# Performance work log

Measured on AMD Instinct MI355X. Metric: run time of the kernel, lower is better.

Reference implementation:

```python
import jax, jax.numpy as jnp
from jax import lax
import numpy as np

D = 512          # dim_embedding
VW = 50000       # word vocab
VC = 256         # char vocab
N = 4096         # number of words
L = 32           # chars per word


def setup_inputs() -> dict:
    key = jax.random.key(0)
    ks = jax.random.split(key, 12)
    inp = {
        "words": jax.random.randint(ks[0], (N,), 0, VW),
        "words_in_char": jax.random.randint(ks[1], (N, L), 0, VC),
        "word_emb": jax.random.normal(ks[2], (VW, D), jnp.float32) * 0.05,
        "chr_emb": jax.random.normal(ks[3], (VC, D), jnp.float32) * 0.05,
        "conv_chr_w": jax.random.normal(ks[4], (D, D, 3), jnp.float32) * 0.02,
        "conv_chr_b": jax.random.normal(ks[5], (D,), jnp.float32) * 0.02,
        "conv_sent_w": jax.random.normal(ks[6], (2 * D, 2 * D, 3), jnp.float32) * 0.02,
        "conv_sent_b": jax.random.normal(ks[7], (2 * D,), jnp.float32) * 0.02,
        "lin1_w": jax.random.normal(ks[8], (4 * D, 2 * D), jnp.float32) * 0.02,
        "lin1_b": jax.random.normal(ks[9], (4 * D,), jnp.float32) * 0.02,
        "lin2_w": jax.random.normal(ks[10], (2, 4 * D), jnp.float32) * 0.02,
        "lin2_b": jax.random.normal(ks[11], (2,), jnp.float32) * 0.02,
    }
    return inp


def reference(words, words_in_char, word_emb, chr_emb, conv_chr_w, conv_chr_b,
              conv_sent_w, conv_sent_b, lin1_w, lin1_b, lin2_w, lin2_b):
    # padding_idx=0 -> row 0 of embeddings is zero
    we = word_emb.at[0].set(0.0)
    ce = chr_emb.at[0].set(0.0)

    n, l = words_in_char.shape
    d = we.shape[1]

    v_word = we[words]                      # [N, D]

    emb_c = ce[words_in_char]               # [N, L, D]
    # FAITHFUL to original: reshape (not transpose) of [L, D] into [D, L]
    x = emb_c.reshape(n, d, l)              # [N, D, L]
    y = lax.conv_general_dilated(
        x, conv_chr_w, window_strides=(1,), padding=[(1, 1)],
        dimension_numbers=("NCH", "OIH", "NCH"))
    y = y + conv_chr_b[None, :, None]       # [N, D, L]
    v_wch = jnp.max(y, axis=2)              # [N, D]  (max-pool over char positions)

    u = jnp.concatenate([v_word, v_wch], axis=1)   # [N, 2D]
    # conv_sentence acts on length-1 sequences with pad=1: only the center
    # kernel tap touches real data -> equivalent to a matmul with w[:, :, 1]
    r = u @ conv_sent_w[:, :, 1].T + conv_sent_b   # [N, 2D]
    r = jnp.max(r, axis=0)                          # [2D] max over words

    h = jnp.tanh(r @ lin1_w.T + lin1_b)             # [4D]
    return h @ lin2_w.T + lin2_b                    # [2]
```

## Files before the change

kernel.cpp:

```cpp
#include <hip/hip_runtime.h>
#include <hip/hip_fp16.h>

typedef _Float16 f16;
typedef __attribute__((ext_vector_type(8))) _Float16 f16x8;
typedef __attribute__((ext_vector_type(4))) float f32x4;

#define WS_CET   0u
#define WS_WC    262144u
#define WS_W1    1835008u
#define WS_U     3932160u
#define WS_PART  12320768u
#define WS_RMAX  12451840u
#define WS_H     12455936u

__global__ __launch_bounds__(512) void k0_ceT(const float* __restrict__ ce,
                                              f16* __restrict__ ceT) {
  int c = blockIdx.x;
  int t = threadIdx.x;
  int m = t >> 5, l = t & 31;
  float v = (c == 0) ? 0.f : ce[c * 512 + m * 32 + l];
  ceT[c * 512 + l * 16 + m] = (f16)v;
}

__global__ __launch_bounds__(256) void k0_wc(const float* __restrict__ w,
                                             f16* __restrict__ Wc) {
  int e = blockIdx.x * 256 + threadIdx.x;
  int k = e >> 18, rem = e & 262143;
  int o = rem >> 9, i = rem & 511;
  Wc[e] = (f16)w[(o * 512 + i) * 3 + k];
}

__global__ __launch_bounds__(256) void k0_w1(const float* __restrict__ w,
                                             f16* __restrict__ W1) {
  int e = blockIdx.x * 256 + threadIdx.x;
  int o = e >> 10, i = e & 1023;
  W1[e] = (f16)w[(o * 1024 + i) * 3 + 1];
}

__global__ __launch_bounds__(256) void k0_u(const int* __restrict__ words,
                                            const float* __restrict__ wemb,
                                            f16* __restrict__ U) {
  int n = blockIdx.x;
  int wd = words[n];
  const float* src = wemb + (size_t)wd * 512;
  for (int i = threadIdx.x; i < 512; i += 256) {
    float v = (wd == 0) ? 0.f : src[i];
    U[n * 1024 + i] = (f16)v;
  }
}

__global__ __launch_bounds__(256) void k1_conv(
    const int* __restrict__ wic, const f16* __restrict__ Wc,
    const f16* __restrict__ ceT, const float* __restrict__ bias,
    f16* __restrict__ U)
{
  __shared__ __align__(16) f16 sA[3 * 128 * 32];
  __shared__ __align__(16) f16 sB[8 * 34 * 32];
  __shared__ int   sChar[256];
  __shared__ float sBias[128];

  const int tid = threadIdx.x;
  const int w0 = blockIdx.x * 8;
  const int o0 = blockIdx.y * 128;
  const int wid = tid >> 6, lane = tid & 63;
  const int wm = wid >> 1, wn = wid & 1;
  const int l15 = lane & 15, g4 = lane >> 4;

  sChar[tid] = wic[w0 * 32 + tid];
  if (tid < 128) sBias[tid] = bias[o0 + tid];

  f32x4 acc[4][8];
#pragma unroll
  for (int m = 0; m < 4; ++m)
#pragma unroll
    for (int n = 0; n < 8; ++n) acc[m][n] = (f32x4){0.f, 0.f, 0.f, 0.f};

  __syncthreads();

  for (int step = 0; step < 16; ++step) {
    const int i0 = step * 32, gb = step * 2;
#pragma unroll
    for (int c = tid; c < 1536; c += 256) {
      int k = c >> 9, rem = c & 511, o = rem >> 2, ch = rem & 3;
      uint4 v = *(const uint4*)(Wc + ((k * 512 + o0 + o) * 512 + i0 + ch * 8));
      *(uint4*)((char*)sA + (((k * 128 + o) * 4 + (ch ^ (o & 3))) << 4)) = v;
    }
    for (int c = tid; c < 1088; c += 256) {
      int w = c / 136, rem = c - w * 136, lp = rem >> 2, ch = rem & 3;
      uint4 v = make_uint4(0u, 0u, 0u, 0u);
      if (lp > 0 && lp < 33) {
        int cc = sChar[(w << 5) + gb + (ch >> 1)];
        v = *(const uint4*)(ceT + (cc * 512 + (lp - 1) * 16 + (ch & 1) * 8));
      }
      *(uint4*)((char*)sB + (((w * 34 + lp) * 4 + (ch ^ (lp & 3))) << 4)) = v;
    }
    __syncthreads();

#pragma unroll
    for (int k = 0; k < 3; ++k) {
      f16x8 a[4];
#pragma unroll
      for (int m = 0; m < 4; ++m) {
        int ol = wm * 64 + m * 16 + l15;
        a[m] = *(const f16x8*)((const char*)sA +
                 (((k * 128 + ol) * 4 + (g4 ^ (ol & 3))) << 4));
      }
#pragma unroll
      for (int n = 0; n < 8; ++n) {
        int w = wn * 4 + (n >> 1);
        int lp = (n & 1) * 16 + l15 + k;
        f16x8 b = *(const f16x8*)((const char*)sB +
                   (((w * 34 + lp) * 4 + (g4 ^ (lp & 3))) << 4));
#pragma unroll
        for (int m = 0; m < 4; ++m)
          acc[m][n] = __builtin_amdgcn_mfma_f32_16x16x32_f16(a[m], b, acc[m][n], 0, 0, 0);
      }
    }
    __syncthreads();
  }

#pragma unroll
  for (int m = 0; m < 4; ++m) {
    float vm[16];
#pragma unroll
    for (int wp = 0; wp < 4; ++wp)
#pragma unroll
      for (int j = 0; j < 4; ++j)
        vm[wp * 4 + j] = fmaxf(acc[m][2 * wp][j], acc[m][2 * wp + 1][j]);
#pragma unroll
    for (int off = 1; off <= 8; off <<= 1)
#pragma unroll
      for (int t = 0; t < 16; ++t)
        vm[t] = fmaxf(vm[t], __shfl_xor(vm[t], off));
    float v = vm[0];
#pragma unroll
    for (int t = 1; t < 16; ++t) v = (l15 == t) ? vm[t] : v;
    int ol = wm * 64 + m * 16 + g4 * 4 + (l15 & 3);
    int word = w0 + wn * 4 + (l15 >> 2);
    U[word * 1024 + 512 + o0 + ol] = (f16)(v + sBias[ol]);
  }
}

__global__ __launch_bounds__(256) void k2_sent(
    const f16* __restrict__ U, const f16* __restrict__ W1,
    float* __restrict__ part)
{
  __shared__ __align__(16) f16 sA[128 * 32];
  __shared__ __align__(16) f16 sB[128 * 32];
  __shared__ float sRed[2][128];

  const int tid = threadIdx.x;
  const int w0 = blockIdx.x * 128;
  const int o0 = blockIdx.y * 128;
  const int wid = tid >> 6, lane = tid & 63;
  const int wm = wid >> 1, wn = wid & 1;
  const int l15 = lane & 15, g4 = lane >> 4;

  f32x4 acc[4][4];
#pragma unroll
  for (int m = 0; m < 4; ++m)
#pragma unroll
    for (int n = 0; n < 4; ++n) acc[m][n] = (f32x4){0.f, 0.f, 0.f, 0.f};

  for (int step = 0; step < 32; ++step) {
    const int i0 = step * 32;
#pragma unroll
    for (int c = tid; c < 512; c += 256) {
      int r = c >> 2, ch = c & 3;
      uint4 va = *(const uint4*)(U + (w0 + r) * 1024 + i0 + ch * 8);
      *(uint4*)((char*)sA + ((r * 4 + (ch ^ (r & 3))) << 4)) = va;
      uint4 vb = *(const uint4*)(W1 + (o0 + r) * 1024 + i0 + ch * 8);
      *(uint4*)((char*)sB + ((r * 4 + (ch ^ (r & 3))) << 4)) = vb;
    }
    __syncthreads();
    f16x8 a[4];
#pragma unroll
    for (int m = 0; m < 4; ++m) {
      int r = wm * 64 + m * 16 + l15;
      a[m] = *(const f16x8*)((const char*)sA + ((r * 4 + (g4 ^ (r & 3))) << 4));
    }
#pragma unroll
    for (int n = 0; n < 4; ++n) {
      int r = wn * 64 + n * 16 + l15;
      f16x8 b = *(const f16x8*)((const char*)sB + ((r * 4 + (g4 ^ (r & 3))) << 4));
#pragma unroll
      for (int m = 0; m < 4; ++m)
        acc[m][n] = __builtin_amdgcn_mfma_f32_16x16x32_f16(a[m], b, acc[m][n], 0, 0, 0);
    }
    __syncthreads();
  }
#pragma unroll
  for (int n = 0; n < 4; ++n) {
    float v = -3.4e38f;
#pragma unroll
    for (int m = 0; m < 4; ++m)
#pragma unroll
      for (int j = 0; j < 4; ++j) v = fmaxf(v, acc[m][n][j]);
    v = fmaxf(v, __shfl_xor(v, 16));
    v = fmaxf(v, __shfl_xor(v, 32));
    if (lane < 16) sRed[wm][wn * 64 + n * 16 + l15] = v;
  }
  __syncthreads();
  if (tid < 128)
    part[blockIdx.x * 1024 + o0 + tid] = fmaxf(sRed[0][tid], sRed[1][tid]);
}

__global__ __launch_bounds__(256) void k3_rmax(const float* __restrict__ part,
                                               const float* __restrict__ sb,
                                               float* __restrict__ rmax) {
  int o = blockIdx.x * 256 + threadIdx.x;
  float v = -3.4e38f;
  for (int r = 0; r < 32; ++r) v = fmaxf(v, part[r * 1024 + o]);
  rmax[o] = v + sb[o];
}

__global__ __launch_bounds__(256) void k3_lin1(const float* __restrict__ w,
                                               const float* __restrict__ b,
                                               const float* __restrict__ rmax,
                                               float* __restrict__ h) {
  __shared__ float sR[1024];
  int tid = threadIdx.x;
  for (int i = tid; i < 1024; i += 256) sR[i] = rmax[i];
  __syncthreads();
  int wid = tid >> 6, lane = tid & 63;
  for (int p = 0; p < 8; ++p) {
    int j = blockIdx.x * 32 + p * 4 + wid;
    float a = 0.f;
    for (int i = lane; i < 1024; i += 64) a += w[j * 1024 + i] * sR[i];
#pragma unroll
    for (int off = 32; off >= 1; off >>= 1) a += __shfl_xor(a, off);
    if (lane == 0) h[j] = tanhf(a + b[j]);
  }
}

__global__ __launch_bounds__(256) void k3_out(const float* __restrict__ h,
                                              const float* __restrict__ w,
                                              const float* __restrict__ b,
                                              float* __restrict__ out) {
  __shared__ float red0[4], red1[4];
  int tid = threadIdx.x, wid = tid >> 6, lane = tid & 63;
  float a0 = 0.f, a1 = 0.f;
  for (int i = tid; i < 2048; i += 256) {
    float hv = h[i];
    a0 += hv * w[i];
    a1 += hv * w[2048 + i];
  }
#pragma unroll
  for (int off = 32; off >= 1; off >>= 1) {
    a0 += __shfl_xor(a0, off);
    a1 += __shfl_xor(a1, off);
  }
  if (lane == 0) { red0[wid] = a0; red1[wid] = a1; }
  __syncthreads();
  if (tid == 0) {
    out[0] = red0[0] + red0[1] + red0[2] + red0[3] + b[0];
    out[1] = red1[0] + red1[1] + red1[2] + red1[3] + b[1];
  }
}

extern "C" void kernel_launch(void* const* d_in, const int* in_sizes, int n_in,
                              void* d_out, int out_size, void* d_ws, size_t ws_size,
                              hipStream_t stream) {
  (void)in_sizes; (void)n_in; (void)out_size; (void)ws_size;
  const int*   words = (const int*)d_in[0];
  const int*   wic   = (const int*)d_in[1];
  const float* wemb  = (const float*)d_in[2];
  const float* cemb  = (const float*)d_in[3];
  const float* ccw   = (const float*)d_in[4];
  const float* ccb   = (const float*)d_in[5];
  const float* csw   = (const float*)d_in[6];
  const float* csb   = (const float*)d_in[7];
  const float* l1w   = (const float*)d_in[8];
  const float* l1b   = (const float*)d_in[9];
  const float* l2w   = (const float*)d_in[10];
  const float* l2b   = (const float*)d_in[11];
  float* out = (float*)d_out;
  char* ws = (char*)d_ws;
  f16* ceT = (f16*)(ws + WS_CET);
  f16* Wc  = (f16*)(ws + WS_WC);
  f16* W1  = (f16*)(ws + WS_W1);
  f16* U   = (f16*)(ws + WS_U);
  float* part = (float*)(ws + WS_PART);
  float* rmax = (float*)(ws + WS_RMAX);
  float* h    = (float*)(ws + WS_H);

  k0_ceT <<<dim3(256),    dim3(512), 0, stream>>>(cemb, ceT);
  k0_wc  <<<dim3(3072),   dim3(256), 0, stream>>>(ccw, Wc);
  k0_w1  <<<dim3(4096),   dim3(256), 0, stream>>>(csw, W1);
  k0_u   <<<dim3(4096),   dim3(256), 0, stream>>>(words, wemb, U);
  k1_conv<<<dim3(512, 4), dim3(256), 0, stream>>>(wic, Wc, ceT, ccb, U);
  k2_sent<<<dim3(32, 8),  dim3(256), 0, stream>>>(U, W1, part);
  k3_rmax<<<dim3(4),      dim3(256), 0, stream>>>(part, csb, rmax);
  k3_lin1<<<dim3(64),     dim3(256), 0, stream>>>(l1w, l1b, rmax, h);
  k3_out <<<dim3(1),      dim3(256), 0, stream>>>(h, l2w, l2b, out);
}
```

Baseline: 709.8 us.

## Fuse prep kernels, double-buffer conv and sentence GEMMs with direct global-to-LDS loads

Merges the four preprocessing kernels into one launch and pre-swizzles the conv weights into a tile-ordered layout. The char-conv kernel now covers 16 words per block with 8x8 MFMA tiles per wave, and the sentence GEMM uses 64-wide K steps. Both GEMMs double-buffer LDS and fill it with global_load_lds, so the next tile's loads overlap the current tile's MFMAs. The cost is more LDS and registers per block (launch bounds now allow one block per SIMD group), which lowers occupancy.

```diff
diff --git a/kernel.cpp b/kernel.cpp
--- a/kernel.cpp
+++ b/kernel.cpp
@@ -13,179 +13,211 @@
 #define WS_RMAX  12451840u
 #define WS_H     12455936u
 
-__global__ __launch_bounds__(512) void k0_ceT(const float* __restrict__ ce,
-                                              f16* __restrict__ ceT) {
-  int c = blockIdx.x;
-  int t = threadIdx.x;
-  int m = t >> 5, l = t & 31;
-  float v = (c == 0) ? 0.f : ce[c * 512 + m * 32 + l];
-  ceT[c * 512 + l * 16 + m] = (f16)v;
-}
-
-__global__ __launch_bounds__(256) void k0_wc(const float* __restrict__ w,
-                                             f16* __restrict__ Wc) {
-  int e = blockIdx.x * 256 + threadIdx.x;
-  int k = e >> 18, rem = e & 262143;
-  int o = rem >> 9, i = rem & 511;
-  Wc[e] = (f16)w[(o * 512 + i) * 3 + k];
-}
-
-__global__ __launch_bounds__(256) void k0_w1(const float* __restrict__ w,
-                                             f16* __restrict__ W1) {
-  int e = blockIdx.x * 256 + threadIdx.x;
-  int o = e >> 10, i = e & 1023;
-  W1[e] = (f16)w[(o * 1024 + i) * 3 + 1];
-}
-
-__global__ __launch_bounds__(256) void k0_u(const int* __restrict__ words,
-                                            const float* __restrict__ wemb,
-                                            f16* __restrict__ U) {
-  int n = blockIdx.x;
-  int wd = words[n];
-  const float* src = wemb + (size_t)wd * 512;
-  for (int i = threadIdx.x; i < 512; i += 256) {
-    float v = (wd == 0) ? 0.f : src[i];
-    U[n * 1024 + i] = (f16)v;
-  }
-}
-
-__global__ __launch_bounds__(256) void k1_conv(
+__device__ __forceinline__ void gload16(const void* g, void* l) {
+  __builtin_amdgcn_global_load_lds(
+      (const __attribute__((address_space(1))) unsigned int*)g,
+      (__attribute__((address_space(3))) unsigned int*)l, 16, 0, 0);
+}
+
+__global__ __launch_bounds__(256) void k0_prep(
+    const int* __restrict__ words, const float* __restrict__ wemb,
+    const float* __restrict__ cemb, const float* __restrict__ ccw,
+    const float* __restrict__ csw,
+    f16* __restrict__ ceT, f16* __restrict__ Wc, f16* __restrict__ W1,
+    f16* __restrict__ U)
+{
+  int b = blockIdx.x, tid = threadIdx.x;
+  if (b < 384) {
+    int q = b * 256 + tid;
+    int oblk = q / 24576;
+    int r = q - oblk * 24576;
+    int step = r / 1536, p = r - step * 1536;
+    int k = p >> 9, ol = (p >> 2) & 127, chp = p & 3;
+    int ch = chp ^ ((ol >> 1) & 3);
+    int o = oblk * 128 + ol, i0 = step * 32 + ch * 8;
+    f16x8 v;
+#pragma unroll
+    for (int j = 0; j < 8; ++j) v[j] = (f16)ccw[(o * 512 + i0 + j) * 3 + k];
+    *(f16x8*)(Wc + (size_t)q * 8) = v;
+  } else if (b < 4480) {
+    int e = (b - 384) * 256 + tid;
+    int o = e >> 10, i = e & 1023;
+    W1[e] = (f16)csw[(o * 1024 + i) * 3 + 1];
+  } else if (b < 4992) {
+    int e = (b - 4480) * 256 + tid;
+    int c = e >> 9, t = e & 511;
+    int m = t >> 5, l = t & 31;
+    float v = (c == 0) ? 0.f : cemb[c * 512 + m * 32 + l];
+    ceT[c * 512 + l * 16 + m] = (f16)v;
+  } else {
+    int n = b - 4992;
+    int wd = words[n];
+    const float* src = wemb + (size_t)wd * 512;
+    for (int i = tid; i < 512; i += 256)
+      U[n * 1024 + i] = (f16)((wd == 0) ? 0.f : src[i]);
+  }
+}
+
+__global__ __launch_bounds__(256, 1) void k1_conv(
     const int* __restrict__ wic, const f16* __restrict__ Wc,
     const f16* __restrict__ ceT, const float* __restrict__ bias,
     f16* __restrict__ U)
 {
-  __shared__ __align__(16) f16 sA[3 * 128 * 32];
-  __shared__ __align__(16) f16 sB[8 * 34 * 32];
-  __shared__ int   sChar[256];
+  __shared__ __align__(16) f16 sA[2][12288];
+  __shared__ __align__(16) f16 sB[2][17408];
+  __shared__ int sChar[512];
   __shared__ float sBias[128];
 
   const int tid = threadIdx.x;
-  const int w0 = blockIdx.x * 8;
-  const int o0 = blockIdx.y * 128;
+  const int w0 = blockIdx.x * 16;
+  const int oblk = blockIdx.y;
+  const int o0 = oblk * 128;
+  const int wid = tid >> 6, lane = tid & 63;
+  const int l15 = lane & 15, g4 = lane >> 4;
+
+  sChar[tid] = wic[w0 * 32 + tid];
+  sChar[tid + 256] = wic[w0 * 32 + 256 + tid];
+  if (tid < 128) sBias[tid] = bias[o0 + tid];
+  {
+    int buf = tid >> 7, rem = tid & 127, w = rem >> 3, q = rem & 7;
+    int chk = w * 136 + (q < 4 ? q : 128 + q);
+    *(uint4*)((char*)sB[buf] + (chk << 4)) = make_uint4(0, 0, 0, 0);
+  }
+  __syncthreads();
+
+  auto stgA = [&](int buf, int step) {
+    const f16* src = Wc + ((size_t)(oblk * 16 + step) * 1536 + wid * 384 + lane) * 8;
+    f16* dst = sA[buf] + wid * 3072;
+#pragma unroll
+    for (int c = 0; c < 6; ++c)
+      gload16(src + c * 512, dst + c * 512);
+  };
+  auto stgB = [&](int buf, int step) {
+#pragma unroll
+    for (int c = 0; c < 8; ++c) {
+      int wl = wid * 4 + (c >> 1), h = c & 1;
+      int lp = 1 + h * 16 + (lane >> 2);
+      int ch = (lane & 3) ^ ((lp >> 1) & 3);
+      int cc = sChar[wl * 32 + step * 2 + (ch >> 1)];
+      gload16(ceT + cc * 512 + (lp - 1) * 16 + (ch & 1) * 8,
+              sB[buf] + (wl * 136 + 4 + h * 64) * 8);
+    }
+  };
+
+  stgA(0, 0); stgB(0, 0);
+
+  f32x4 acc[8][8];
+#pragma unroll
+  for (int m = 0; m < 8; ++m)
+#pragma unroll
+    for (int n = 0; n < 8; ++n) acc[m][n] = (f32x4){0.f, 0.f, 0.f, 0.f};
+
+  __syncthreads();
+
+  for (int t = 0; t < 16; ++t) {
+    const int cur = t & 1;
+    if (t < 15) { stgA(cur ^ 1, t + 1); stgB(cur ^ 1, t + 1); }
+    const f16* A = sA[cur];
+    const f16* B = sB[cur];
+#pragma unroll
+    for (int k = 0; k < 3; ++k) {
+      f16x8 a[8];
+#pragma unroll
+      for (int m = 0; m < 8; ++m) {
+        int row = m * 16 + l15;
+        int pc = g4 ^ ((row >> 1) & 3);
+        a[m] = *(const f16x8*)(A + ((k * 128 + row) * 4 + pc) * 8);
+      }
+#pragma unroll
+      for (int n = 0; n < 8; ++n) {
+        int wl = wid * 4 + (n >> 1);
+        int lp = (n & 1) * 16 + l15 + k;
+        int pc = g4 ^ ((lp >> 1) & 3);
+        f16x8 bfr = *(const f16x8*)(B + (wl * 136 + lp * 4 + pc) * 8);
+#pragma unroll
+        for (int m = 0; m < 8; ++m)
+          acc[m][n] = __builtin_amdgcn_mfma_f32_16x16x32_f16(a[m], bfr, acc[m][n], 0, 0, 0);
+      }
+    }
+    __syncthreads();
+  }
+
+#pragma unroll
+  for (int m = 0; m < 8; ++m) {
+    float vm[16];
+#pragma unroll
+    for (int wp = 0; wp < 4; ++wp)
+#pragma unroll
+      for (int j = 0; j < 4; ++j)
+        vm[wp * 4 + j] = fmaxf(acc[m][2 * wp][j], acc[m][2 * wp + 1][j]);
+#pragma unroll
+    for (int off = 1; off <= 8; off <<= 1)
+#pragma unroll
+      for (int q = 0; q < 16; ++q)
+        vm[q] = fmaxf(vm[q], __shfl_xor(vm[q], off));
+    float v = vm[0];
+#pragma unroll
+    for (int q = 1; q < 16; ++q) v = (l15 == q) ? vm[q] : v;
+    int ol = m * 16 + g4 * 4 + (l15 & 3);
+    int word = w0 + wid * 4 + (l15 >> 2);
+    U[word * 1024 + 512 + o0 + ol] = (f16)(v + sBias[ol]);
+  }
+}
+
+__global__ __launch_bounds__(256, 1) void k2_sent(
+    const f16* __restrict__ U, const f16* __restrict__ W1,
+    float* __restrict__ part)
+{
+  __shared__ __align__(16) f16 sA[2][8192];
+  __shared__ __align__(16) f16 sB[2][8192];
+  __shared__ float sRed[2][128];
+
+  const int tid = threadIdx.x;
+  const int w0 = blockIdx.x * 128, o0 = blockIdx.y * 128;
   const int wid = tid >> 6, lane = tid & 63;
   const int wm = wid >> 1, wn = wid & 1;
   const int l15 = lane & 15, g4 = lane >> 4;
 
-  sChar[tid] = wic[w0 * 32 + tid];
-  if (tid < 128) sBias[tid] = bias[o0 + tid];
-
-  f32x4 acc[4][8];
+  auto stg = [&](int buf, int step) {
+    int i0 = step * 64;
+#pragma unroll
+    for (int c = 0; c < 4; ++c) {
+      int row = wid * 32 + c * 8 + (lane >> 3);
+      int ch = (lane & 7) ^ (row & 7);
+      gload16(U  + (size_t)(w0 + row) * 1024 + i0 + ch * 8, sA[buf] + (wid * 32 + c * 8) * 64);
+      gload16(W1 + (size_t)(o0 + row) * 1024 + i0 + ch * 8, sB[buf] + (wid * 32 + c * 8) * 64);
+    }
+  };
+
+  stg(0, 0);
+  f32x4 acc[4][4];
 #pragma unroll
   for (int m = 0; m < 4; ++m)
 #pragma unroll
-    for (int n = 0; n < 8; ++n) acc[m][n] = (f32x4){0.f, 0.f, 0.f, 0.f};
-
-  __syncthreads();
-
-  for (int step = 0; step < 16; ++step) {
-    const int i0 = step * 32, gb = step * 2;
-#pragma unroll
-    for (int c = tid; c < 1536; c += 256) {
-      int k = c >> 9, rem = c & 511, o = rem >> 2, ch = rem & 3;
-      uint4 v = *(const uint4*)(Wc + ((k * 512 + o0 + o) * 512 + i0 + ch * 8));
-      *(uint4*)((char*)sA + (((k * 128 + o) * 4 + (ch ^ (o & 3))) << 4)) = v;
-    }
-    for (int c = tid; c < 1088; c += 256) {
-      int w = c / 136, rem = c - w * 136, lp = rem >> 2, ch = rem & 3;
-      uint4 v = make_uint4(0u, 0u, 0u, 0u);
-      if (lp > 0 && lp < 33) {
-        int cc = sChar[(w << 5) + gb + (ch >> 1)];
-        v = *(const uint4*)(ceT + (cc * 512 + (lp - 1) * 16 + (ch & 1) * 8));
+    for (int n = 0; n < 4; ++n) acc[m][n] = (f32x4){0.f, 0.f, 0.f, 0.f};
+  __syncthreads();
+
+  for (int t = 0; t < 16; ++t) {
+    const int cur = t & 1;
+    if (t < 15) stg(cur ^ 1, t + 1);
+#pragma unroll
+    for (int s = 0; s < 2; ++s) {
+      f16x8 a[4];
+#pragma unroll
+      for (int m = 0; m < 4; ++m) {
+        int row = wm * 64 + m * 16 + l15;
+        int pc = (s * 4 + g4) ^ (row & 7);
+        a[m] = *(const f16x8*)(sA[cur] + row * 64 + pc * 8);
       }
-      *(uint4*)((char*)sB + (((w * 34 + lp) * 4 + (ch ^ (lp & 3))) << 4)) = v;
-    }
-    __syncthreads();
-
-#pragma unroll
-    for (int k = 0; k < 3; ++k) {
-      f16x8 a[4];
-#pragma unroll
-      for (int m = 0; m < 4; ++m) {
-        int ol = wm * 64 + m * 16 + l15;
-        a[m] = *(const f16x8*)((const char*)sA +
-                 (((k * 128 + ol) * 4 + (g4 ^ (ol & 3))) << 4));
+#pragma unroll
+      for (int n = 0; n < 4; ++n) {
+        int row = wn * 64 + n * 16 + l15;
+        int pc = (s * 4 + g4) ^ (row & 7);
+        f16x8 bfr = *(const f16x8*)(sB[cur] + row * 64 + pc * 8);
+#pragma unroll
+        for (int m = 0; m < 4; ++m)
+          acc[m][n] = __builtin_amdgcn_mfma_f32_16x16x32_f16(a[m], bfr, acc[m][n], 0, 0, 0);
       }
-#pragma unroll
-      for (int n = 0; n < 8; ++n) {
-        int w = wn * 4 + (n >> 1);
-        int lp = (n & 1) * 16 + l15 + k;
-        f16x8 b = *(const f16x8*)((const char*)sB +
-                   (((w * 34 + lp) * 4 + (g4 ^ (lp & 3))) << 4));
-#pragma unroll
-        for (int m = 0; m < 4; ++m)
-          acc[m][n] = __builtin_amdgcn_mfma_f32_16x16x32_f16(a[m], b, acc[m][n], 0, 0, 0);
-      }
-    }
-    __syncthreads();
-  }
-
-#pragma unroll
-  for (int m = 0; m < 4; ++m) {
-    float vm[16];
-#pragma unroll
-    for (int wp = 0; wp < 4; ++wp)
-#pragma unroll
-      for (int j = 0; j < 4; ++j)
-        vm[wp * 4 + j] = fmaxf(acc[m][2 * wp][j], acc[m][2 * wp + 1][j]);
-#pragma unroll
-    for (int off = 1; off <= 8; off <<= 1)
-#pragma unroll
-      for (int t = 0; t < 16; ++t)
-        vm[t] = fmaxf(vm[t], __shfl_xor(vm[t], off));
-    float v = vm[0];
-#pragma unroll
-    for (int t = 1; t < 16; ++t) v = (l15 == t) ? vm[t] : v;
-    int ol = wm * 64 + m * 16 + g4 * 4 + (l15 & 3);
-    int word = w0 + wn * 4 + (l15 >> 2);
-    U[word * 1024 + 512 + o0 + ol] = (f16)(v + sBias[ol]);
-  }
-}
-
-__global__ __launch_bounds__(256) void k2_sent(
-    const f16* __restrict__ U, const f16* __restrict__ W1,
-    float* __restrict__ part)
-{
-  __shared__ __align__(16) f16 sA[128 * 32];
-  __shared__ __align__(16) f16 sB[128 * 32];
-  __shared__ float sRed[2][128];
-
-  const int tid = threadIdx.x;
-  const int w0 = blockIdx.x * 128;
-  const int o0 = blockIdx.y * 128;
-  const int wid = tid >> 6, lane = tid & 63;
-  const int wm = wid >> 1, wn = wid & 1;
-  const int l15 = lane & 15, g4 = lane >> 4;
-
-  f32x4 acc[4][4];
-#pragma unroll
-  for (int m = 0; m < 4; ++m)
-#pragma unroll
-    for (int n = 0; n < 4; ++n) acc[m][n] = (f32x4){0.f, 0.f, 0.f, 0.f};
-
-  for (int step = 0; step < 32; ++step) {
-    const int i0 = step * 32;
-#pragma unroll
-    for (int c = tid; c < 512; c += 256) {
-      int r = c >> 2, ch = c & 3;
-      uint4 va = *(const uint4*)(U + (w0 + r) * 1024 + i0 + ch * 8);
-      *(uint4*)((char*)sA + ((r * 4 + (ch ^ (r & 3))) << 4)) = va;
-      uint4 vb = *(const uint4*)(W1 + (o0 + r) * 1024 + i0 + ch * 8);
-      *(uint4*)((char*)sB + ((r * 4 + (ch ^ (r & 3))) << 4)) = vb;
-    }
-    __syncthreads();
-    f16x8 a[4];
-#pragma unroll
-    for (int m = 0; m < 4; ++m) {
-      int r = wm * 64 + m * 16 + l15;
-      a[m] = *(const f16x8*)((const char*)sA + ((r * 4 + (g4 ^ (r & 3))) << 4));
-    }
-#pragma unroll
-    for (int n = 0; n < 4; ++n) {
-      int r = wn * 64 + n * 16 + l15;
-      f16x8 b = *(const f16x8*)((const char*)sB + ((r * 4 + (g4 ^ (r & 3))) << 4));
-#pragma unroll
-      for (int m = 0; m < 4; ++m)
-        acc[m][n] = __builtin_amdgcn_mfma_f32_16x16x32_f16(a[m], b, acc[m][n], 0, 0, 0);
     }
     __syncthreads();
   }
@@ -284,11 +316,9 @@
   float* rmax = (float*)(ws + WS_RMAX);
   float* h    = (float*)(ws + WS_H);
 
-  k0_ceT <<<dim3(256),    dim3(512), 0, stream>>>(cemb, ceT);
-  k0_wc  <<<dim3(3072),   dim3(256), 0, stream>>>(ccw, Wc);
-  k0_w1  <<<dim3(4096),   dim3(256), 0, stream>>>(csw, W1);
-  k0_u   <<<dim3(4096),   dim3(256), 0, stream>>>(words, wemb, U);
-  k1_conv<<<dim3(512, 4), dim3(256), 0, stream>>>(wic, Wc, ceT, ccb, U);
+  k0_prep<<<dim3(9088),   dim3(256), 0, stream>>>(words, wemb, cemb, ccw, csw,
+                                                  ceT, Wc, W1, U);
+  k1_conv<<<dim3(256, 4), dim3(256), 0, stream>>>(wic, Wc, ceT, ccb, U);
   k2_sent<<<dim3(32, 8),  dim3(256), 0, stream>>>(U, W1, part);
   k3_rmax<<<dim3(4),      dim3(256), 0, stream>>>(part, csb, rmax);
   k3_lin1<<<dim3(64),     dim3(256), 0, stream>>>(l1w, l1b, rmax, h);
```

Result: faster. 633.4 us (-10.8%).
